# Optimization experiments

Hardware: AMD Instinct MI355X
Metric: run time of the kernel (lower is better)

The kernel has to match this reference:

```python
import jax, jax.numpy as jnp
import numpy as np

NUM_EMB = 100000
EMB = 64
NUM_CTNS = 10
HEADS = 4
ATT = 32
HD = HEADS * ATT  # 128
FIELDS = 32       # 20 onehot + 2 multihot + 10 ctns
B = 8192


def _linear_params(key, out_f, in_f):
    kw, kb = jax.random.split(key)
    W = jax.random.normal(kw, (out_f, in_f), jnp.float32) * 0.05
    b = jax.random.normal(kb, (out_f,), jnp.float32) * 0.05
    return W, b


def setup_inputs() -> dict:
    key = jax.random.key(0)
    ks = jax.random.split(key, 16)
    inp = {
        'onehot_i': jax.random.randint(ks[0], (B, 20), 0, NUM_EMB),
        'onehot_x': jax.random.uniform(ks[1], (B, 20), jnp.float32),
        'mh_i': jax.random.randint(ks[2], (2, B, 50), 0, NUM_EMB),
        'mh_x': jax.random.uniform(ks[3], (2, B, 50), jnp.float32),
        'ctns': jax.random.normal(ks[4], (B, NUM_CTNS), jnp.float32),
        'xx': jax.random.normal(ks[5], (NUM_EMB, EMB), jnp.float32),
        'xy': jax.random.normal(ks[6], (NUM_CTNS, EMB), jnp.float32),
    }
    # layer 1 attention params (emb -> h*d)
    names1 = ['QW1', 'Qb1', 'KW1', 'Kb1', 'VW1', 'Vb1', 'RW1', 'Rb1']
    for i in range(4):
        W, b = _linear_params(ks[7 + i], HD, EMB)
        inp[names1[2 * i]] = W
        inp[names1[2 * i + 1]] = b
    # layer 2 attention params (h*d -> h*d)
    names2 = ['QW2', 'Qb2', 'KW2', 'Kb2', 'VW2', 'Vb2', 'RW2', 'Rb2']
    for i in range(4):
        W, b = _linear_params(ks[11 + i], HD, HD)
        inp[names2[2 * i]] = W
        inp[names2[2 * i + 1]] = b
    lW, lb = _linear_params(ks[15], 1, FIELDS * HD)
    inp['logitW'] = lW
    inp['logitb'] = lb
    return inp


def _attn_block(y, QW, Qb, KW, Kb, VW, Vb, RW, Rb):
    # y: [B, F, D]; heads are head-major in the h*d output dim (matches torch split/cat)
    b, f, _ = y.shape
    Q = (y @ QW.T + Qb).reshape(b, f, HEADS, ATT)
    K = (y @ KW.T + Kb).reshape(b, f, HEADS, ATT)
    V = (y @ VW.T + Vb).reshape(b, f, HEADS, ATT)
    Res = y @ RW.T + Rb
    scores = jnp.einsum('bqhd,bkhd->bhqk', Q, K)  # unscaled, as in source
    A = jax.nn.softmax(scores, axis=-1)
    O = jnp.einsum('bhqk,bkhd->bqhd', A, V).reshape(b, f, HD)
    return jax.nn.relu(O + Res)


def reference(onehot_i, onehot_x, mh_i, mh_x, ctns, xx, xy,
              QW1, Qb1, KW1, Kb1, VW1, Vb1, RW1, Rb1,
              QW2, Qb2, KW2, Kb2, VW2, Vb2, RW2, Rb2,
              logitW, logitb):
    onehot_fields = xx[onehot_i] * onehot_x[..., None]                 # [B,20,EMB]
    mh_fields = (xx[mh_i] * mh_x[..., None]).sum(axis=2)               # [2,B,EMB]
    mh_fields = jnp.transpose(mh_fields, (1, 0, 2))                    # [B,2,EMB]
    ctns_fields = ctns[..., None] * xy                                 # [B,10,EMB]
    y = jnp.concatenate([onehot_fields, mh_fields, ctns_fields], axis=1)  # [B,32,EMB]
    y = _attn_block(y, QW1, Qb1, KW1, Kb1, VW1, Vb1, RW1, Rb1)
    y = _attn_block(y, QW2, Qb2, KW2, Kb2, VW2, Vb2, RW2, Rb2)
    flat = y.reshape(y.shape[0], -1)                                   # [B, 32*128]
    out = jax.nn.sigmoid(flat @ logitW.T + logitb)
    return out.squeeze()
```

## Files before the change

### kernel.cpp

```cpp
#include <hip/hip_runtime.h>
#include <hip/hip_bf16.h>


#define NSAMP 8192
#define S_Y1 72
#define S_T 36

typedef __attribute__((ext_vector_type(8))) short bf8_t;
typedef __attribute__((ext_vector_type(16))) float f16v;

__device__ __forceinline__ short f2bf(float f) {
  unsigned u = __float_as_uint(f);
  u += 0x7fffu + ((u >> 16) & 1u);
  return (short)(u >> 16);
}
__device__ __forceinline__ unsigned pack2(float a, float b) {
  __hip_bfloat162 h = __float22bfloat162_rn(float2{a, b});
  union { __hip_bfloat162 h2; unsigned u; } cvt;
  cvt.h2 = h;
  return cvt.u;
}
__device__ __forceinline__ float bf2f(short s) {
  return __uint_as_float(((unsigned)(unsigned short)s) << 16);
}
__device__ __forceinline__ float rcp_fast(float x) {
  return __builtin_amdgcn_rcpf(x);
}
__device__ __forceinline__ f16v mfma32(bf8_t a, bf8_t b, f16v c) {
  return __builtin_amdgcn_mfma_f32_32x32x16_bf16(a, b, c, 0, 0, 0);
}

template<int KS, bool HAS_NEXT>
__device__ __forceinline__ void projPF(const bf8_t (&af)[2][KS],
                                       const short* __restrict__ W,
                                       const float* __restrict__ bias,
                                       int fragBase,
                                       const short* __restrict__ Wnext,
                                       int fbNext, int n0, int col,
                                       bf8_t (&pre)[4], f16v (&o)[2]) {
  constexpr int PF = (KS < 4) ? KS : 4;
  bf8_t nxt[4];
  if constexpr (HAS_NEXT) {
#pragma unroll
    for (int i = 0; i < 4; ++i)
      nxt[i] = *(const bf8_t*)&Wnext[fbNext + i * 512];
  }
  float bb = bias[n0 + col];
#pragma unroll
  for (int i = 0; i < 16; ++i) { o[0][i] = bb; o[1][i] = bb; }
#pragma unroll
  for (int kc = 0; kc < KS; ++kc) {
    bf8_t w;
    if (kc < PF) w = pre[kc];
    else w = *(const bf8_t*)&W[fragBase + kc * 512];
    o[0] = mfma32(af[0][kc], w, o[0]);
    o[1] = mfma32(af[1][kc], w, o[1]);
  }
  if constexpr (HAS_NEXT) {
#pragma unroll
    for (int i = 0; i < 4; ++i) pre[i] = nxt[i];
  }
}

__device__ __forceinline__ void storeQuad(short* tile, int stride, int g, int h2,
                                          int col, float a0, float a1, float a2,
                                          float a3) {
  unsigned p01 = pack2(a0, a1);
  unsigned p23 = pack2(a2, a3);
  int rb = 8 * g + 4 * h2;
  tile[(rb + 0) * stride + col] = (short)(p01 & 0xffffu);
  tile[(rb + 1) * stride + col] = (short)(p01 >> 16);
  tile[(rb + 2) * stride + col] = (short)(p23 & 0xffffu);
  tile[(rb + 3) * stride + col] = (short)(p23 >> 16);
}

template<int D_IN, bool FUSE>
__device__ void attn_layer(const short* yIn0, const short* yIn1,
                           short* yOut0, short* yOut1,
                           const short* __restrict__ Wq, const short* __restrict__ Wk,
                           const short* __restrict__ Wv, const short* __restrict__ Wr,
                           const float* __restrict__ bq, const float* __restrict__ bk,
                           const float* __restrict__ bvp, const float* __restrict__ br,
                           short* bQ0, short* bK0, short* bQ1, short* bK1,
                           const short* __restrict__ lwF,
                           const short* __restrict__ WnlQ, int fbNext,
                           int n0, int col, int h2, bf8_t (&pre)[4],
                           float (&pp)[2]) {
  constexpr int KS = D_IN / 16;
  const short* yIn[2] = {yIn0, yIn1};
  short* bQ[2] = {bQ0, bQ1};
  short* bK[2] = {bK0, bK1};
  const int head = n0 >> 5;
  const int lane = h2 * 32 + col;
  const int fragBase = head * KS * 512 + lane * 8;

  bf8_t af[2][KS];
#pragma unroll
  for (int sp = 0; sp < 2; ++sp)
#pragma unroll
    for (int kc = 0; kc < KS; ++kc) {
      if constexpr (FUSE) {
        int gsw = (kc * 2 + h2) ^ (col & 15);
        af[sp][kc] = *(const bf8_t*)&yIn[sp][col * 128 + (gsw << 3)];
      } else {
        af[sp][kc] = *(const bf8_t*)&yIn[sp][col * S_Y1 + kc * 16 + h2 * 8];
      }
    }
  if constexpr (!FUSE)
    __syncthreads();

  f16v acc[2];

  projPF<KS, true>(af, Wq, bq, fragBase, Wk, fragBase, n0, col, pre, acc);
#pragma unroll
  for (int sp = 0; sp < 2; ++sp)
#pragma unroll
    for (int g = 0; g < 4; ++g)
      storeQuad(bQ[sp], S_T, g, h2, col, acc[sp][4 * g + 0], acc[sp][4 * g + 1],
                acc[sp][4 * g + 2], acc[sp][4 * g + 3]);

  projPF<KS, true>(af, Wk, bk, fragBase, Wr, fragBase, n0, col, pre, acc);
#pragma unroll
  for (int sp = 0; sp < 2; ++sp)
#pragma unroll
    for (int g = 0; g < 4; ++g)
      storeQuad(bK[sp], S_T, g, h2, col, acc[sp][4 * g + 0], acc[sp][4 * g + 1],
                acc[sp][4 * g + 2], acc[sp][4 * g + 3]);

  f16v res[2];
  projPF<KS, true>(af, Wr, br, fragBase, Wv, fragBase, n0, col, pre, res);

#pragma unroll
  for (int sp = 0; sp < 2; ++sp) {
    f16v z;
#pragma unroll
    for (int i = 0; i < 16; ++i) z[i] = 0.f;
#pragma unroll
    for (int kc = 0; kc < 2; ++kc) {
      bf8_t qa = *(const bf8_t*)&bQ[sp][col * S_T + kc * 16 + h2 * 8];
      bf8_t kb = *(const bf8_t*)&bK[sp][col * S_T + kc * 16 + h2 * 8];
      z = mfma32(qa, kb, z);
    }
#pragma unroll
    for (int g = 0; g < 4; ++g)
      storeQuad(bQ[sp], S_T, g, h2, col,
                __expf(z[4 * g + 0]), __expf(z[4 * g + 1]),
                __expf(z[4 * g + 2]), __expf(z[4 * g + 3]));
  }

  projPF<KS, !FUSE>(af, Wv, bvp, fragBase, WnlQ, fbNext, n0, col, pre, acc);
#pragma unroll
  for (int sp = 0; sp < 2; ++sp)
#pragma unroll
    for (int g = 0; g < 4; ++g) {
      uint2 pk;
      pk.x = pack2(acc[sp][g * 4 + 0], acc[sp][g * 4 + 1]);
      pk.y = pack2(acc[sp][g * 4 + 2], acc[sp][g * 4 + 3]);
      *(uint2*)&bK[sp][col * S_T + 8 * g + 4 * h2] = pk;
    }

  short4 l4b[4];
  if constexpr (FUSE) {
#pragma unroll
    for (int g = 0; g < 4; ++g)
      l4b[g] = *(const short4*)&lwF[(head * 4 + g) * 256 + lane * 4];
  }

  const short onebf = (short)0x3F80;
  bf8_t ones = {onebf, onebf, onebf, onebf, onebf, onebf, onebf, onebf};
  f16v pv[2], sums[2];
#pragma unroll
  for (int sp = 0; sp < 2; ++sp) {
#pragma unroll
    for (int i = 0; i < 16; ++i) { pv[sp][i] = 0.f; sums[sp][i] = 0.f; }
#pragma unroll
    for (int kc = 0; kc < 2; ++kc) {
      bf8_t pa = *(const bf8_t*)&bQ[sp][col * S_T + kc * 16 + h2 * 8];
      bf8_t vb = *(const bf8_t*)&bK[sp][col * S_T + kc * 16 + h2 * 8];
      pv[sp] = mfma32(pa, vb, pv[sp]);
      sums[sp] = mfma32(pa, ones, sums[sp]);
    }
  }

  if constexpr (FUSE) {
#pragma unroll
    for (int g = 0; g < 4; ++g) {
      short4 l4 = l4b[g];
#pragma unroll
      for (int r = 0; r < 4; ++r) {
        int reg = g * 4 + r;
        float lw = bf2f((r == 0) ? l4.x : (r == 1) ? l4.y : (r == 2) ? l4.z : l4.w);
        pp[0] += fmaxf(fmaf(pv[0][reg], rcp_fast(sums[0][reg]), res[0][reg]), 0.f) * lw;
        pp[1] += fmaxf(fmaf(pv[1][reg], rcp_fast(sums[1][reg]), res[1][reg]), 0.f) * lw;
      }
    }
  } else {
    short* yOut[2] = {yOut0, yOut1};
    const int cg = head * 4 + (col >> 3);
    const int cw = col & 7;
#pragma unroll
    for (int sp = 0; sp < 2; ++sp)
#pragma unroll
      for (int g = 0; g < 4; ++g) {
        float v[4];
#pragma unroll
        for (int r = 0; r < 4; ++r)
          v[r] = fmaxf(fmaf(pv[sp][4 * g + r], rcp_fast(sums[sp][4 * g + r]),
                            res[sp][4 * g + r]), 0.f);
        unsigned p01 = pack2(v[0], v[1]);
        unsigned p23 = pack2(v[2], v[3]);
        int rb = 8 * g + 4 * h2;
        short s4[4] = {(short)(p01 & 0xffffu), (short)(p01 >> 16),
                       (short)(p23 & 0xffffu), (short)(p23 >> 16)};
#pragma unroll
        for (int r = 0; r < 4; ++r) {
          int row = rb + r;
          yOut[sp][row * 128 + ((cg ^ (row & 15)) << 3) + cw] = s4[r];
        }
      }
  }
}

__global__ __launch_bounds__(256, 3) void autoint_main(
    const int* __restrict__ onehot_i, const float* __restrict__ onehot_x,
    const int* __restrict__ mh_i, const float* __restrict__ mh_x,
    const float* __restrict__ ctns, const float* __restrict__ xx,
    const float* __restrict__ xy,
    const float* __restrict__ bq1, const float* __restrict__ bk1,
    const float* __restrict__ bv1, const float* __restrict__ br1,
    const float* __restrict__ bq2, const float* __restrict__ bk2,
    const float* __restrict__ bv2, const float* __restrict__ br2,
    const float* __restrict__ logitb, const short* __restrict__ wbf,
    float* __restrict__ out) {
  __shared__ __align__(16) short scr[2][9216];
  __shared__ __align__(16) short y2s[2][4096];

  const int t = threadIdx.x;
  const int head = t >> 6;
  const int lane = t & 63;
  const int col = lane & 31;
  const int h2 = lane >> 5;
  const int n0 = head * 32;
  const int s0 = blockIdx.x * 2;

  short* bQ0 = &scr[0][(head * 2 + 0) * 1152];
  short* bK0 = &scr[0][(head * 2 + 1) * 1152];
  short* bQ1 = &scr[1][(head * 2 + 0) * 1152];
  short* bK1 = &scr[1][(head * 2 + 1) * 1152];

  const int fb1 = head * 4 * 512 + lane * 8;
  const int fb2 = head * 8 * 512 + lane * 8;
  bf8_t pre[4];
#pragma unroll
  for (int i = 0; i < 4; ++i) pre[i] = *(const bf8_t*)&wbf[fb1 + i * 512];

  const int e4 = t & 15, f0 = t >> 4;

  int oh_r[2][2]; float oh_w[2][2];
#pragma unroll
  for (int se = 0; se < 2; ++se) {
    oh_r[0][se] = onehot_i[(s0 + se) * 20 + f0];
    oh_w[0][se] = onehot_x[(s0 + se) * 20 + f0];
  }
  if (t < 64) {
#pragma unroll
    for (int se = 0; se < 2; ++se) {
      oh_r[1][se] = onehot_i[(s0 + se) * 20 + 16 + f0];
      oh_w[1][se] = onehot_x[(s0 + se) * 20 + 16 + f0];
    }
  }
  if (t < 160) {
    int ci = t >> 4;
    float4 xv = *(const float4*)&xy[ci * 64 + e4 * 4];
    float cv0 = ctns[(s0 + 0) * 10 + ci];
    float cv1 = ctns[(s0 + 1) * 10 + ci];
    uint2 w0; w0.x = pack2(cv0 * xv.x, cv0 * xv.y); w0.y = pack2(cv0 * xv.z, cv0 * xv.w);
    *(uint2*)&scr[0][(22 + ci) * S_Y1 + e4 * 4] = w0;
    uint2 w1; w1.x = pack2(cv1 * xv.x, cv1 * xv.y); w1.y = pack2(cv1 * xv.z, cv1 * xv.w);
    *(uint2*)&scr[1][(22 + ci) * S_Y1 + e4 * 4] = w1;
  }

  float4 g0[2], g1[2];
#pragma unroll
  for (int se = 0; se < 2; ++se)
    g0[se] = *(const float4*)&xx[oh_r[0][se] * 64 + e4 * 4];
  if (t < 64) {
#pragma unroll
    for (int se = 0; se < 2; ++se)
      g1[se] = *(const float4*)&xx[oh_r[1][se] * 64 + e4 * 4];
  }

  {
    const int slot = t >> 3, ks = t & 7;
    const int j = slot >> 4, e4m = slot & 15;
#pragma unroll
    for (int se = 0; se < 2; ++se) {
      const int sg = s0 + se;
      const int* ip = &mh_i[(j * NSAMP + sg) * 50];
      const float* xp = &mh_x[(j * NSAMP + sg) * 50];
      int rw[7]; float wt[7];
#pragma unroll
      for (int i = 0; i < 7; ++i) {
        int k = ks + 8 * i;
        int ok = (k < 50);
        rw[i] = ok ? ip[k] : 0;
        wt[i] = ok ? xp[k] : 0.f;
      }
      float4 xv[7];
#pragma unroll
      for (int i = 0; i < 7; ++i)
        xv[i] = *(const float4*)&xx[rw[i] * 64 + e4m * 4];
      float a0 = 0.f, a1 = 0.f, a2 = 0.f, a3 = 0.f;
#pragma unroll
      for (int i = 0; i < 7; ++i) {
        a0 += xv[i].x * wt[i]; a1 += xv[i].y * wt[i];
        a2 += xv[i].z * wt[i]; a3 += xv[i].w * wt[i];
      }
#pragma unroll
      for (int d = 1; d < 8; d <<= 1) {
        a0 += __shfl_xor(a0, d); a1 += __shfl_xor(a1, d);
        a2 += __shfl_xor(a2, d); a3 += __shfl_xor(a3, d);
      }
      if (ks == 0) {
        uint2 w; w.x = pack2(a0, a1); w.y = pack2(a2, a3);
        *(uint2*)&scr[se][(20 + j) * S_Y1 + e4m * 4] = w;
      }
    }
  }

#pragma unroll
  for (int se = 0; se < 2; ++se) {
    float xw = oh_w[0][se];
    uint2 w; w.x = pack2(g0[se].x * xw, g0[se].y * xw);
    w.y = pack2(g0[se].z * xw, g0[se].w * xw);
    *(uint2*)&scr[se][f0 * S_Y1 + e4 * 4] = w;
  }
  if (t < 64) {
#pragma unroll
    for (int se = 0; se < 2; ++se) {
      float xw = oh_w[1][se];
      uint2 w; w.x = pack2(g1[se].x * xw, g1[se].y * xw);
      w.y = pack2(g1[se].z * xw, g1[se].w * xw);
      *(uint2*)&scr[se][(16 + f0) * S_Y1 + e4 * 4] = w;
    }
  }
  __syncthreads();

  float pp[2] = {0.f, 0.f};
  attn_layer<64, false>(&scr[0][0], &scr[1][0], &y2s[0][0], &y2s[1][0],
      wbf + 0, wbf + 8192, wbf + 16384, wbf + 24576,
      bq1, bk1, bv1, br1, bQ0, bK0, bQ1, bK1, nullptr,
      wbf + 32768, fb2, n0, col, h2, pre, pp);
  __syncthreads();
  attn_layer<128, true>(&y2s[0][0], &y2s[1][0], nullptr, nullptr,
      wbf + 32768, wbf + 49152, wbf + 65536, wbf + 81920,
      bq2, bk2, bv2, br2, bQ0, bK0, bQ1, bK1, wbf + 98304,
      wbf, 0, n0, col, h2, pre, pp);

  float* red0 = (float*)bQ0;
  float* red1 = (float*)bQ1;
#pragma unroll
  for (int off = 32; off > 0; off >>= 1) {
    pp[0] += __shfl_xor(pp[0], off);
    pp[1] += __shfl_xor(pp[1], off);
  }
  if (lane == 0) { red0[0] = pp[0]; red1[0] = pp[1]; }
  __syncthreads();
  if (t < 2) {
    const short* base = t == 0 ? &scr[0][0] : &scr[1][0];
    float zz = logitb[0];
#pragma unroll
    for (int h = 0; h < 4; ++h)
      zz += *(const float*)&base[(h * 2) * 1152];
    out[s0 + t] = 1.f / (1.f + __expf(-zz));
  }
}

__global__ void convert_w(const float* __restrict__ qw1, const float* __restrict__ kw1,
                          const float* __restrict__ vw1, const float* __restrict__ rw1,
                          const float* __restrict__ qw2, const float* __restrict__ kw2,
                          const float* __restrict__ vw2, const float* __restrict__ rw2,
                          const float* __restrict__ lw, short* __restrict__ outw) {
  int i = blockIdx.x * 256 + threadIdx.x;
  if (i >= 102400) return;
  float v;
  if (i < 32768) {
    int tsel = i >> 13, d = i & 8191;
    int e = d & 7, lane = (d >> 3) & 63, kc = (d >> 9) & 3, h = (d >> 11) & 3;
    int col = lane & 31, h2 = lane >> 5;
    int j = (h * 32 + col) * 64 + kc * 16 + h2 * 8 + e;
    const float* src = tsel == 0 ? qw1 : tsel == 1 ? kw1 : tsel == 2 ? vw1 : rw1;
    v = src[j];
  } else if (i < 98304) {
    int k = i - 32768;
    int tsel = k >> 14, d = k & 16383;
    int e = d & 7, lane = (d >> 3) & 63, kc = (d >> 9) & 7, h = (d >> 12) & 3;
    int col = lane & 31, h2 = lane >> 5;
    int j = (h * 32 + col) * 128 + kc * 16 + h2 * 8 + e;
    const float* src = tsel == 0 ? qw2 : tsel == 1 ? kw2 : tsel == 2 ? vw2 : rw2;
    v = src[j];
  } else {
    int d = i - 98304;
    int r = d & 3, lane = (d >> 2) & 63, g = (d >> 8) & 3, h = (d >> 10) & 3;
    int col = lane & 31, h2 = lane >> 5;
    v = lw[(8 * g + 4 * h2 + r) * 128 + h * 32 + col];
  }
  outw[i] = f2bf(v);
}

extern "C" void kernel_launch(void* const* d_in, const int* in_sizes, int n_in,
                              void* d_out, int out_size, void* d_ws, size_t ws_size,
                              hipStream_t stream) {
  short* wbf = (short*)d_ws;
  convert_w<<<400, 256, 0, stream>>>(
      (const float*)d_in[7], (const float*)d_in[9], (const float*)d_in[11],
      (const float*)d_in[13], (const float*)d_in[15], (const float*)d_in[17],
      (const float*)d_in[19], (const float*)d_in[21], (const float*)d_in[23], wbf);
  autoint_main<<<NSAMP / 2, 256, 0, stream>>>(
      (const int*)d_in[0], (const float*)d_in[1], (const int*)d_in[2],
      (const float*)d_in[3], (const float*)d_in[4], (const float*)d_in[5],
      (const float*)d_in[6],
      (const float*)d_in[8], (const float*)d_in[10], (const float*)d_in[12],
      (const float*)d_in[14], (const float*)d_in[16], (const float*)d_in[18],
      (const float*)d_in[20], (const float*)d_in[22], (const float*)d_in[24],
      wbf, (float*)d_out);
}
```

Baseline: 242.3 us.

## Keep Q, K and softmax probabilities in registers via swapped MFMA and lane shuffles

Q and K projections are computed with the MFMA operands swapped, so the outputs come out transposed. Lane-exchange shuffles then turn those outputs directly into bf16 A/B fragments for the score MFMA. The exponentiated scores are also rebuilt in registers as the P fragment, so only V goes through shared memory. This removes the scalar LDS stores and reloads of Q, K and P, halves the scratch LDS footprint, and reorders V before R so the V store overlaps the R projection. In exchange it adds shuffle and pack instructions and raises register pressure, which may hurt occupancy under the 3-blocks-per-SM launch bound.

```diff
diff --git a/kernel.cpp b/kernel.cpp
--- a/kernel.cpp
+++ b/kernel.cpp
@@ -28,6 +28,31 @@
 }
 __device__ __forceinline__ f16v mfma32(bf8_t a, bf8_t b, f16v c) {
   return __builtin_amdgcn_mfma_f32_32x32x16_bf16(a, b, c, 0, 0, 0);
+}
+
+__device__ __forceinline__ bf8_t xchg(unsigned a01, unsigned a23,
+                                      unsigned b01, unsigned b23, int h2) {
+  unsigned pa01 = (unsigned)__shfl_xor((int)a01, 32);
+  unsigned pa23 = (unsigned)__shfl_xor((int)a23, 32);
+  unsigned pb01 = (unsigned)__shfl_xor((int)b01, 32);
+  unsigned pb23 = (unsigned)__shfl_xor((int)b23, 32);
+  union { bf8_t v; unsigned u[4]; } r;
+  r.u[0] = h2 ? pb01 : a01;
+  r.u[1] = h2 ? pb23 : a23;
+  r.u[2] = h2 ? b01 : pa01;
+  r.u[3] = h2 ? b23 : pa23;
+  return r.v;
+}
+
+__device__ __forceinline__ void buildFrag(const f16v& o, int h2, bf8_t (&dst)[2]) {
+#pragma unroll
+  for (int kc = 0; kc < 2; ++kc) {
+    unsigned a01 = pack2(o[8 * kc + 0], o[8 * kc + 1]);
+    unsigned a23 = pack2(o[8 * kc + 2], o[8 * kc + 3]);
+    unsigned b01 = pack2(o[8 * kc + 4], o[8 * kc + 5]);
+    unsigned b23 = pack2(o[8 * kc + 6], o[8 * kc + 7]);
+    dst[kc] = xchg(a01, a23, b01, b23, h2);
+  }
 }
 
 template<int KS, bool HAS_NEXT>
@@ -62,16 +87,41 @@
   }
 }
 
-__device__ __forceinline__ void storeQuad(short* tile, int stride, int g, int h2,
-                                          int col, float a0, float a1, float a2,
-                                          float a3) {
-  unsigned p01 = pack2(a0, a1);
-  unsigned p23 = pack2(a2, a3);
-  int rb = 8 * g + 4 * h2;
-  tile[(rb + 0) * stride + col] = (short)(p01 & 0xffffu);
-  tile[(rb + 1) * stride + col] = (short)(p01 >> 16);
-  tile[(rb + 2) * stride + col] = (short)(p23 & 0xffffu);
-  tile[(rb + 3) * stride + col] = (short)(p23 >> 16);
+template<int KS, bool HAS_NEXT>
+__device__ __forceinline__ void projSwp(const bf8_t (&af)[2][KS],
+                                        const short* __restrict__ W,
+                                        const float* __restrict__ bias,
+                                        int fragBase,
+                                        const short* __restrict__ Wnext,
+                                        int fbNext, int n0, int h2,
+                                        bf8_t (&pre)[4], f16v (&o)[2]) {
+  constexpr int PF = (KS < 4) ? KS : 4;
+  bf8_t nxt[4];
+  if constexpr (HAS_NEXT) {
+#pragma unroll
+    for (int i = 0; i < 4; ++i)
+      nxt[i] = *(const bf8_t*)&Wnext[fbNext + i * 512];
+  }
+#pragma unroll
+  for (int g = 0; g < 4; ++g) {
+    float4 b4 = *(const float4*)&bias[n0 + 8 * g + 4 * h2];
+    o[0][4 * g + 0] = b4.x; o[0][4 * g + 1] = b4.y;
+    o[0][4 * g + 2] = b4.z; o[0][4 * g + 3] = b4.w;
+    o[1][4 * g + 0] = b4.x; o[1][4 * g + 1] = b4.y;
+    o[1][4 * g + 2] = b4.z; o[1][4 * g + 3] = b4.w;
+  }
+#pragma unroll
+  for (int kc = 0; kc < KS; ++kc) {
+    bf8_t w;
+    if (kc < PF) w = pre[kc];
+    else w = *(const bf8_t*)&W[fragBase + kc * 512];
+    o[0] = mfma32(w, af[0][kc], o[0]);
+    o[1] = mfma32(w, af[1][kc], o[1]);
+  }
+  if constexpr (HAS_NEXT) {
+#pragma unroll
+    for (int i = 0; i < 4; ++i) pre[i] = nxt[i];
+  }
 }
 
 template<int D_IN, bool FUSE>
@@ -81,15 +131,14 @@
                            const short* __restrict__ Wv, const short* __restrict__ Wr,
                            const float* __restrict__ bq, const float* __restrict__ bk,
                            const float* __restrict__ bvp, const float* __restrict__ br,
-                           short* bQ0, short* bK0, short* bQ1, short* bK1,
+                           short* bV0, short* bV1,
                            const short* __restrict__ lwF,
                            const short* __restrict__ WnlQ, int fbNext,
                            int n0, int col, int h2, bf8_t (&pre)[4],
                            float (&pp)[2]) {
   constexpr int KS = D_IN / 16;
   const short* yIn[2] = {yIn0, yIn1};
-  short* bQ[2] = {bQ0, bQ1};
-  short* bK[2] = {bK0, bK1};
+  short* bV[2] = {bV0, bV1};
   const int head = n0 >> 5;
   const int lane = h2 * 32 + col;
   const int fragBase = head * KS * 512 + lane * 8;
@@ -106,49 +155,23 @@
         af[sp][kc] = *(const bf8_t*)&yIn[sp][col * S_Y1 + kc * 16 + h2 * 8];
       }
     }
+
+  f16v acc[2];
+  bf8_t afq[2][2], afk[2][2];
+
+  projSwp<KS, true>(af, Wq, bq, fragBase, Wk, fragBase, n0, h2, pre, acc);
+  buildFrag(acc[0], h2, afq[0]);
+  buildFrag(acc[1], h2, afq[1]);
+
+  projSwp<KS, true>(af, Wk, bk, fragBase, Wv, fragBase, n0, h2, pre, acc);
+  buildFrag(acc[0], h2, afk[0]);
+  buildFrag(acc[1], h2, afk[1]);
+
+  projPF<KS, true>(af, Wv, bvp, fragBase, Wr, fragBase, n0, col, pre, acc);
+
   if constexpr (!FUSE)
     __syncthreads();
 
-  f16v acc[2];
-
-  projPF<KS, true>(af, Wq, bq, fragBase, Wk, fragBase, n0, col, pre, acc);
-#pragma unroll
-  for (int sp = 0; sp < 2; ++sp)
-#pragma unroll
-    for (int g = 0; g < 4; ++g)
-      storeQuad(bQ[sp], S_T, g, h2, col, acc[sp][4 * g + 0], acc[sp][4 * g + 1],
-                acc[sp][4 * g + 2], acc[sp][4 * g + 3]);
-
-  projPF<KS, true>(af, Wk, bk, fragBase, Wr, fragBase, n0, col, pre, acc);
-#pragma unroll
-  for (int sp = 0; sp < 2; ++sp)
-#pragma unroll
-    for (int g = 0; g < 4; ++g)
-      storeQuad(bK[sp], S_T, g, h2, col, acc[sp][4 * g + 0], acc[sp][4 * g + 1],
-                acc[sp][4 * g + 2], acc[sp][4 * g + 3]);
-
-  f16v res[2];
-  projPF<KS, true>(af, Wr, br, fragBase, Wv, fragBase, n0, col, pre, res);
-
-#pragma unroll
-  for (int sp = 0; sp < 2; ++sp) {
-    f16v z;
-#pragma unroll
-    for (int i = 0; i < 16; ++i) z[i] = 0.f;
-#pragma unroll
-    for (int kc = 0; kc < 2; ++kc) {
-      bf8_t qa = *(const bf8_t*)&bQ[sp][col * S_T + kc * 16 + h2 * 8];
-      bf8_t kb = *(const bf8_t*)&bK[sp][col * S_T + kc * 16 + h2 * 8];
-      z = mfma32(qa, kb, z);
-    }
-#pragma unroll
-    for (int g = 0; g < 4; ++g)
-      storeQuad(bQ[sp], S_T, g, h2, col,
-                __expf(z[4 * g + 0]), __expf(z[4 * g + 1]),
-                __expf(z[4 * g + 2]), __expf(z[4 * g + 3]));
-  }
-
-  projPF<KS, !FUSE>(af, Wv, bvp, fragBase, WnlQ, fbNext, n0, col, pre, acc);
 #pragma unroll
   for (int sp = 0; sp < 2; ++sp)
 #pragma unroll
@@ -156,8 +179,30 @@
       uint2 pk;
       pk.x = pack2(acc[sp][g * 4 + 0], acc[sp][g * 4 + 1]);
       pk.y = pack2(acc[sp][g * 4 + 2], acc[sp][g * 4 + 3]);
-      *(uint2*)&bK[sp][col * S_T + 8 * g + 4 * h2] = pk;
-    }
+      *(uint2*)&bV[sp][col * S_T + 8 * g + 4 * h2] = pk;
+    }
+
+  f16v res[2];
+  projPF<KS, !FUSE>(af, Wr, br, fragBase, WnlQ, fbNext, n0, col, pre, res);
+
+  f16v z[2];
+#pragma unroll
+  for (int sp = 0; sp < 2; ++sp) {
+#pragma unroll
+    for (int i = 0; i < 16; ++i) z[sp][i] = 0.f;
+#pragma unroll
+    for (int kc = 0; kc < 2; ++kc)
+      z[sp] = mfma32(afk[sp][kc], afq[sp][kc], z[sp]);
+  }
+
+  bf8_t pa[2][2];
+#pragma unroll
+  for (int sp = 0; sp < 2; ++sp) {
+    f16v e;
+#pragma unroll
+    for (int i = 0; i < 16; ++i) e[i] = __expf(z[sp][i]);
+    buildFrag(e, h2, pa[sp]);
+  }
 
   short4 l4b[4];
   if constexpr (FUSE) {
@@ -175,10 +220,9 @@
     for (int i = 0; i < 16; ++i) { pv[sp][i] = 0.f; sums[sp][i] = 0.f; }
 #pragma unroll
     for (int kc = 0; kc < 2; ++kc) {
-      bf8_t pa = *(const bf8_t*)&bQ[sp][col * S_T + kc * 16 + h2 * 8];
-      bf8_t vb = *(const bf8_t*)&bK[sp][col * S_T + kc * 16 + h2 * 8];
-      pv[sp] = mfma32(pa, vb, pv[sp]);
-      sums[sp] = mfma32(pa, ones, sums[sp]);
+      bf8_t vb = *(const bf8_t*)&bV[sp][col * S_T + kc * 16 + h2 * 8];
+      pv[sp] = mfma32(pa[sp][kc], vb, pv[sp]);
+      sums[sp] = mfma32(pa[sp][kc], ones, sums[sp]);
     }
   }
 
@@ -232,7 +276,7 @@
     const float* __restrict__ bv2, const float* __restrict__ br2,
     const float* __restrict__ logitb, const short* __restrict__ wbf,
     float* __restrict__ out) {
-  __shared__ __align__(16) short scr[2][9216];
+  __shared__ __align__(16) short scr[2][4608];
   __shared__ __align__(16) short y2s[2][4096];
 
   const int t = threadIdx.x;
@@ -243,10 +287,8 @@
   const int n0 = head * 32;
   const int s0 = blockIdx.x * 2;
 
-  short* bQ0 = &scr[0][(head * 2 + 0) * 1152];
-  short* bK0 = &scr[0][(head * 2 + 1) * 1152];
-  short* bQ1 = &scr[1][(head * 2 + 0) * 1152];
-  short* bK1 = &scr[1][(head * 2 + 1) * 1152];
+  short* bV0 = &scr[0][head * 1152];
+  short* bV1 = &scr[1][head * 1152];
 
   const int fb1 = head * 4 * 512 + lane * 8;
   const int fb2 = head * 8 * 512 + lane * 8;
@@ -349,16 +391,16 @@
   float pp[2] = {0.f, 0.f};
   attn_layer<64, false>(&scr[0][0], &scr[1][0], &y2s[0][0], &y2s[1][0],
       wbf + 0, wbf + 8192, wbf + 16384, wbf + 24576,
-      bq1, bk1, bv1, br1, bQ0, bK0, bQ1, bK1, nullptr,
+      bq1, bk1, bv1, br1, bV0, bV1, nullptr,
       wbf + 32768, fb2, n0, col, h2, pre, pp);
   __syncthreads();
   attn_layer<128, true>(&y2s[0][0], &y2s[1][0], nullptr, nullptr,
       wbf + 32768, wbf + 49152, wbf + 65536, wbf + 81920,
-      bq2, bk2, bv2, br2, bQ0, bK0, bQ1, bK1, wbf + 98304,
+      bq2, bk2, bv2, br2, bV0, bV1, wbf + 98304,
       wbf, 0, n0, col, h2, pre, pp);
 
-  float* red0 = (float*)bQ0;
-  float* red1 = (float*)bQ1;
+  float* red0 = (float*)bV0;
+  float* red1 = (float*)bV1;
 #pragma unroll
   for (int off = 32; off > 0; off >>= 1) {
     pp[0] += __shfl_xor(pp[0], off);
@@ -371,7 +413,7 @@
     float zz = logitb[0];
 #pragma unroll
     for (int h = 0; h < 4; ++h)
-      zz += *(const float*)&base[(h * 2) * 1152];
+      zz += *(const float*)&base[h * 1152];
     out[s0 + t] = 1.f / (1.f + __expf(-zz));
   }
 }
```

After: 265.6 us. +9.6%, slower.
